# Kernel tuning notes

Measured on AMD Instinct MI355X. Metric: run time of the kernel, lower is better.

The kernel has to match this reference:

```python
import jax, jax.numpy as jnp
import numpy as np

N = 100_000      # total nodes in batched graph
NE = 800_000     # total edges
G = 1_000        # number of graphs in batch
V_DIM = 128      # node feat dim (== H_DIM, required by GRUCell usage)
E_DIM = 64       # edge feat dim
H_DIM = 128      # hidden dim
K_HEAD = 4       # multi-scale interaction heads


def _leaky(x):
    return jnp.where(x >= 0, x, 0.1 * x)


def _gru_cell(x, h, Wih, Whh, bih, bhh):
    # torch nn.GRUCell math; Wih/Whh stored as [in, 3*h] with (r,z,n) chunk order
    gi = x @ Wih + bih
    gh = h @ Whh + bhh
    ir, iz, inn = jnp.split(gi, 3, axis=-1)
    hr, hz, hn = jnp.split(gh, 3, axis=-1)
    r = jax.nn.sigmoid(ir + hr)
    z = jax.nn.sigmoid(iz + hz)
    n = jnp.tanh(inn + r * hn)
    return (1.0 - z) * n + z * h


def setup_inputs() -> dict:
    key = jax.random.key(0)
    ks = iter(jax.random.split(key, 48))
    def rn(shape, scale=0.05):
        return (jax.random.normal(next(ks), shape) * scale).astype(jnp.float32)
    inp = {}
    inp["v"] = rn((N, V_DIM), 1.0)
    inp["e"] = rn((NE, E_DIM), 1.0)
    inp["s"] = rn((G, V_DIM), 1.0)
    inp["edge_src"] = jax.random.randint(next(ks), (NE,), 0, N)
    inp["edge_dst"] = jax.random.randint(next(ks), (NE,), 0, N)
    inp["node_graph"] = jnp.repeat(jnp.arange(G), N // G)  # sorted segment ids
    # top-level linears (stored [in, out])
    inp["A_w"] = rn((V_DIM, H_DIM)); inp["A_b"] = rn((H_DIM,))
    inp["mA_w"] = rn((K_HEAD, V_DIM, H_DIM)); inp["mA_b"] = rn((K_HEAD, H_DIM))
    inp["mB_w"] = rn((K_HEAD, V_DIM, H_DIM)); inp["mB_b"] = rn((K_HEAD, H_DIM))
    inp["mC_w"] = rn((K_HEAD, H_DIM)); inp["mC_b"] = rn((K_HEAD,))
    inp["mD_w"] = rn((K_HEAD, V_DIM, H_DIM)); inp["mD_b"] = rn((K_HEAD, H_DIM))
    inp["B_w"] = rn((H_DIM * K_HEAD, H_DIM)); inp["B_b"] = rn((H_DIM,))
    inp["C_w"] = rn((V_DIM, H_DIM)); inp["C_b"] = rn((H_DIM,))
    inp["K_w"] = rn((E_DIM, H_DIM)); inp["K_b"] = rn((H_DIM,))
    inp["E_w"] = rn((H_DIM + V_DIM, H_DIM)); inp["E_b"] = rn((H_DIM,))
    for pfx in ("gm", "gs"):
        inp[pfx + "_A_w"] = rn((H_DIM, H_DIM)); inp[pfx + "_A_b"] = rn((H_DIM,))
        inp[pfx + "_B_w"] = rn((H_DIM, H_DIM)); inp[pfx + "_B_b"] = rn((H_DIM,))
        inp[pfx + "_Wih"] = rn((H_DIM, 3 * H_DIM)); inp[pfx + "_Whh"] = rn((H_DIM, 3 * H_DIM))
        inp[pfx + "_bih"] = rn((3 * H_DIM,)); inp[pfx + "_bhh"] = rn((3 * H_DIM,))
    return inp


def reference(v, e, s, edge_src, edge_dst, node_graph,
              A_w, A_b, mA_w, mA_b, mB_w, mB_b, mC_w, mC_b, mD_w, mD_b,
              B_w, B_b, C_w, C_b, K_w, K_b, E_w, E_b,
              gm_A_w, gm_A_b, gm_B_w, gm_B_b, gm_Wih, gm_Whh, gm_bih, gm_bhh,
              gs_A_w, gs_A_b, gs_B_w, gs_B_b, gs_Wih, gs_Whh, gs_bih, gs_bhh):
    # super -> super
    s2s = jnp.tanh(s @ A_w + A_b)                                       # [G,H]
    # multi-head node->super attention pooling (Multi_scale_interaction)
    d_node = jnp.tanh(jnp.einsum('nv,kvh->knh', v, mA_w) + mA_b[:, None, :])     # [K,N,H]
    d_super = jnp.tanh(jnp.einsum('gv,kvh->kgh', s, mB_w) + mB_b[:, None, :])    # [K,G,H]
    a = jnp.einsum('knh,kh->nk', d_node * d_super[:, node_graph, :], mC_w) + mC_b[None, :]  # [N,K]
    a_max = jax.ops.segment_max(a, node_graph, num_segments=G, indices_are_sorted=True)
    a_exp = jnp.exp(a - a_max[node_graph])
    denom = jax.ops.segment_sum(a_exp, node_graph, num_segments=G, indices_are_sorted=True)
    attn = a_exp / denom[node_graph]                                    # per-graph softmax, [N,K]
    d_v = jnp.einsum('nv,kvh->nkh', v, mD_w) + mD_b[None, :, :]         # [N,K,H]
    pooled = jax.ops.segment_sum(d_v * attn[:, :, None], node_graph, num_segments=G,
                                 indices_are_sorted=True)               # [G,K,H]
    m2s = jnp.tanh(pooled.reshape(G, K_HEAD * H_DIM) @ B_w + B_b)       # [G,H]
    # super -> node broadcast
    s2m = jnp.tanh(s @ C_w + C_b)[node_graph]                           # [N,H]
    # edge-wise message: leaky_relu(K(e) * v_src) summed into destination node
    ve = _leaky((e @ K_w + K_b) * v[edge_src])                          # [E,H]
    sve = jax.ops.segment_sum(ve, edge_dst, num_segments=N)             # [N,H]
    m2m = _leaky(jnp.concatenate([sve, v], axis=1) @ E_w + E_b)         # [N,H]
    # adaptive GRU gate: node update
    z_m = jax.nn.sigmoid(m2m @ gm_A_w + gm_A_b + s2m @ gm_B_w + gm_B_b)
    h_m = z_m * s2m + (1.0 - z_m) * m2m
    update_v = _gru_cell(v, h_m, gm_Wih, gm_Whh, gm_bih, gm_bhh)
    # adaptive GRU gate: supernode update
    z_s = jax.nn.sigmoid(s2s @ gs_A_w + gs_A_b + m2s @ gs_B_w + gs_B_b)
    h_s = z_s * m2s + (1.0 - z_s) * s2s
    update_s = _gru_cell(s, h_s, gs_Wih, gs_Whh, gs_bih, gs_bhh)
    return (update_v, update_s)
```

## Files before the change

### kernel.cpp

```cpp
#include <hip/hip_runtime.h>

#define NN   100000
#define NEDG 800000
#define NG   1000
#define HD   128
#define EDIM 64

typedef unsigned short u16;
typedef __bf16 bf16x8 __attribute__((ext_vector_type(8)));
typedef float f32x4 __attribute__((ext_vector_type(4)));

#define MFMA16(a, b, c) __builtin_amdgcn_mfma_f32_16x16x32_bf16(a, b, c, 0, 0, 0)

#define WS_E    0
#define WS_GA   4096
#define WS_WIH  6144
#define WS_WHH  12288
#define WS_MA0  18432
#define WS_KW   26624
#define WS_LANES 27648

#define BF(base, NTT, ks, nt, lane) \
    (*(const bf16x8*)(wsw + (size_t)((base) + (((ks) * (NTT) + (nt)) * 64 + (lane))) * 8))

__device__ __forceinline__ float sigmoidf_(float x) { return 1.0f / (1.0f + __expf(-x)); }
__device__ __forceinline__ float tanhf_(float x) {
    float ax = fabsf(x);
    float e  = __expf(-2.0f * ax);
    float t  = (1.0f - e) / (1.0f + e);
    return copysignf(t, x);
}
__device__ __forceinline__ float leaky_(float x) { return x >= 0.f ? x : 0.1f * x; }
__device__ __forceinline__ u16 f2bf(float x) {
    union { float f; unsigned u; } c; c.f = x;
    unsigned r = c.u + 0x7FFF + ((c.u >> 16) & 1);
    return (u16)(r >> 16);
}

__device__ __forceinline__ void stg4(u16* lds, int P, int r, int c0, float4 v4) {
    int byteoff = (c0 << 1) ^ ((r & 7) << 4);
    u16* p = lds + r * P + (byteoff >> 1);
    p[0] = f2bf(v4.x); p[1] = f2bf(v4.y); p[2] = f2bf(v4.z); p[3] = f2bf(v4.w);
}
__device__ __forceinline__ void stg1(u16* lds, int P, int r, int c, u16 val) {
    int byteoff = (c << 1) ^ ((r & 7) << 4);
    lds[r * P + (byteoff >> 1)] = val;
}
__device__ __forceinline__ bf16x8 ldA(const u16* lds, int P, int r, int ks, int hi) {
    int byteoff = (ks * 64 + (hi << 4)) ^ ((r & 7) << 4);
    return *(const bf16x8*)(lds + r * P + (byteoff >> 1));
}

__global__ __launch_bounds__(256) void wconv(
    const float* __restrict__ E_w, const float* __restrict__ gmA_w,
    const float* __restrict__ Wih, const float* __restrict__ Whh,
    const float* __restrict__ mA_w, const float* __restrict__ K_w,
    u16* __restrict__ dst)
{
    int t = blockIdx.x * 256 + threadIdx.x;
    if (t >= WS_LANES) return;
    const float* W; int N; int local;
    if (t < 4096)       { W = E_w;  N = 128; local = t; }
    else if (t < 6144)  { W = gmA_w; N = 128; local = t - 4096; }
    else if (t < 12288) { W = Wih;  N = 384; local = t - 6144; }
    else if (t < 18432) { W = Whh;  N = 384; local = t - 12288; }
    else if (t < 26624) { int k = (t - 18432) >> 11; W = mA_w + k * 128 * 128; N = 128; local = (t - 18432) & 2047; }
    else                { W = K_w;  N = 128; local = t - 26624; }
    int lane = local & 63;
    int fid  = local >> 6;
    int NT = N >> 4;
    int ks = fid / NT, nt = fid - ks * NT;
    int krow = ks * 32 + ((lane >> 4) << 3);
    int col  = nt * 16 + (lane & 15);
    u16* d = dst + (size_t)t * 8;
    #pragma unroll
    for (int j = 0; j < 8; j++) d[j] = f2bf(W[(size_t)(krow + j) * N + col]);
}

__global__ __launch_bounds__(128) void k1_graph(
    const float* __restrict__ s,
    const float* __restrict__ A_w, const float* __restrict__ A_b,
    const float* __restrict__ mB_w, const float* __restrict__ mB_b,
    const float* __restrict__ mC_w,
    const float* __restrict__ C_w, const float* __restrict__ C_b,
    const float* __restrict__ gmB_w, const float* __restrict__ gmA_b, const float* __restrict__ gmB_b,
    float* __restrict__ s2s, float* __restrict__ wkg,
    float* __restrict__ s2m_tab, float* __restrict__ t2)
{
    __shared__ float sm[HD];
    __shared__ float sm2[HD];
    const int g = blockIdx.x, t = threadIdx.x;
    sm[t] = s[g * HD + t];
    __syncthreads();
    {
        float a = 0.f;
        #pragma unroll 8
        for (int i = 0; i < HD; i++) a = fmaf(sm[i], A_w[i * HD + t], a);
        s2s[g * HD + t] = tanhf_(a + A_b[t]);
    }
    for (int k = 0; k < 4; k++) {
        float a = 0.f;
        const float* W = mB_w + k * HD * HD;
        #pragma unroll 8
        for (int i = 0; i < HD; i++) a = fmaf(sm[i], W[i * HD + t], a);
        float d = tanhf_(a + mB_b[k * HD + t]);
        wkg[(k * NG + g) * HD + t] = d * mC_w[k * HD + t];
    }
    float s2m;
    {
        float a = 0.f;
        #pragma unroll 8
        for (int i = 0; i < HD; i++) a = fmaf(sm[i], C_w[i * HD + t], a);
        s2m = tanhf_(a + C_b[t]);
        s2m_tab[g * HD + t] = s2m;
    }
    sm2[t] = s2m;
    __syncthreads();
    {
        float a = 0.f;
        #pragma unroll 8
        for (int i = 0; i < HD; i++) a = fmaf(sm2[i], gmB_w[i * HD + t], a);
        t2[g * HD + t] = a + gmA_b[t] + gmB_b[t];
    }
}

__global__ __launch_bounds__(256) void k2_ascore(
    const float* __restrict__ v, const int* __restrict__ ngr,
    const u16* __restrict__ wsw,
    const float* __restrict__ mA_b, const float* __restrict__ mC_b,
    const float* __restrict__ wkg,
    float* __restrict__ aexp, float* __restrict__ denom)
{
    __shared__ u16 VT[64 * 128];
    const int tid = threadIdx.x;
    const int n0 = blockIdx.x * 64;
    #pragma unroll
    for (int l = 0; l < 8; l++) {
        int i = tid + 256 * l;
        int r = i >> 5, c0 = (i & 31) << 2;
        int node = n0 + r;
        float4 vv = (node < NN) ? *(const float4*)(v + (size_t)node * HD + c0)
                                : make_float4(0.f, 0.f, 0.f, 0.f);
        stg4(VT, 128, r, c0, vv);
    }
    __syncthreads();
    const int lane = tid & 63, w = tid >> 6;
    const int l15 = lane & 15, hi = lane >> 4;
    const int rbase = w * 16;
    bf16x8 av[4];
    #pragma unroll
    for (int ks = 0; ks < 4; ks++) av[ks] = ldA(VT, 128, rbase + l15, ks, hi);
    int gq[4], nodeq[4];
    #pragma unroll
    for (int q = 0; q < 4; q++) {
        int nd = n0 + rbase + hi * 4 + q;
        nodeq[q] = nd;
        gq[q] = ngr[min(nd, NN - 1)];
    }
    for (int k = 0; k < 4; k++) {
        float rs[4] = {0.f, 0.f, 0.f, 0.f};
        const float* bias = mA_b + k * HD;
        #pragma unroll
        for (int nt = 0; nt < 8; nt++) {
            f32x4 acc = {0.f, 0.f, 0.f, 0.f};
            #pragma unroll
            for (int ks = 0; ks < 4; ks++)
                acc = MFMA16(av[ks], BF(WS_MA0 + k * 2048, 8, ks, nt, lane), acc);
            int col = nt * 16 + l15;
            float bb = bias[col];
            #pragma unroll
            for (int q = 0; q < 4; q++)
                rs[q] += tanhf_(acc[q] + bb) * wkg[((size_t)k * NG + gq[q]) * HD + col];
        }
        #pragma unroll
        for (int q = 0; q < 4; q++) {
            float x = rs[q];
            x += __shfl_xor(x, 1); x += __shfl_xor(x, 2);
            x += __shfl_xor(x, 4); x += __shfl_xor(x, 8);
            if (l15 == 0 && nodeq[q] < NN) {
                float ev = __expf(x + mC_b[k]);
                aexp[(size_t)nodeq[q] * 4 + k] = ev;
                atomicAdd(&denom[gq[q] * 4 + k], ev);
            }
        }
    }
}

__global__ __launch_bounds__(256) void k3_edge(
    const float* __restrict__ e, const float* __restrict__ v,
    const int* __restrict__ esrc, const int* __restrict__ edst,
    const u16* __restrict__ wsw, const float* __restrict__ K_b,
    float* __restrict__ sve)
{
    __shared__ u16 ET[64 * 64];
    const int tid = threadIdx.x;
    const int e0 = blockIdx.x * 64;
    #pragma unroll
    for (int l = 0; l < 4; l++) {
        int i = tid + 256 * l;
        int r = i >> 4, c0 = (i & 15) << 2;
        float4 ev4 = *(const float4*)(e + (size_t)(e0 + r) * EDIM + c0);
        stg4(ET, 64, r, c0, ev4);
    }
    __syncthreads();
    const int lane = tid & 63, w = tid >> 6;
    const int l15 = lane & 15, hi = lane >> 4;
    const int rbase = w * 16;
    bf16x8 ae[2];
    #pragma unroll
    for (int ks = 0; ks < 2; ks++) ae[ks] = ldA(ET, 64, rbase + l15, ks, hi);
    int sq[4], dq[4];
    #pragma unroll
    for (int q = 0; q < 4; q++) {
        int ei = e0 + rbase + hi * 4 + q;
        sq[q] = esrc[ei]; dq[q] = edst[ei];
    }
    #pragma unroll
    for (int nt = 0; nt < 8; nt++) {
        f32x4 acc = {0.f, 0.f, 0.f, 0.f};
        acc = MFMA16(ae[0], BF(WS_KW, 8, 0, nt, lane), acc);
        acc = MFMA16(ae[1], BF(WS_KW, 8, 1, nt, lane), acc);
        int col = nt * 16 + l15;
        float kb = K_b[col];
        #pragma unroll
        for (int q = 0; q < 4; q++) {
            float val = (acc[q] + kb) * v[(size_t)sq[q] * HD + col];
            val = leaky_(val);
            atomicAdd(&sve[(size_t)dq[q] * HD + col], val);
        }
    }
}

__global__ __launch_bounds__(256) void k4_vbar(
    const float* __restrict__ v, const int* __restrict__ ngr,
    const float* __restrict__ aexp, const float* __restrict__ denom,
    float* __restrict__ vbar)
{
    const int tid = threadIdx.x;
    const int d = tid & 127;
    const int hf = tid >> 7;
    const int n0 = blockIdx.x * 32 + hf * 16;
    int gcur = -1;
    float a0 = 0.f, a1 = 0.f, a2 = 0.f, a3 = 0.f;
    float4 rd = make_float4(0.f, 0.f, 0.f, 0.f);
    for (int nd = 0; nd < 16; nd++) {
        int n = n0 + nd;
        int g = ngr[n];
        if (g != gcur) {
            if (gcur >= 0) {
                atomicAdd(&vbar[(gcur * 4 + 0) * HD + d], a0);
                atomicAdd(&vbar[(gcur * 4 + 1) * HD + d], a1);
                atomicAdd(&vbar[(gcur * 4 + 2) * HD + d], a2);
                atomicAdd(&vbar[(gcur * 4 + 3) * HD + d], a3);
                a0 = a1 = a2 = a3 = 0.f;
            }
            float4 dn = *(const float4*)&denom[g * 4];
            rd = make_float4(1.f / dn.x, 1.f / dn.y, 1.f / dn.z, 1.f / dn.w);
            gcur = g;
        }
        float4 ae = *(const float4*)&aexp[n * 4];
        float vv = v[(size_t)n * HD + d];
        a0 = fmaf(ae.x * rd.x, vv, a0);
        a1 = fmaf(ae.y * rd.y, vv, a1);
        a2 = fmaf(ae.z * rd.z, vv, a2);
        a3 = fmaf(ae.w * rd.w, vv, a3);
    }
    atomicAdd(&vbar[(gcur * 4 + 0) * HD + d], a0);
    atomicAdd(&vbar[(gcur * 4 + 1) * HD + d], a1);
    atomicAdd(&vbar[(gcur * 4 + 2) * HD + d], a2);
    atomicAdd(&vbar[(gcur * 4 + 3) * HD + d], a3);
}

__global__ __launch_bounds__(128) void k5_super(
    const float* __restrict__ s, const float* __restrict__ vbar,
    const float* __restrict__ mD_w, const float* __restrict__ mD_b,
    const float* __restrict__ B_w, const float* __restrict__ B_b,
    const float* __restrict__ s2s,
    const float* __restrict__ gsA_w, const float* __restrict__ gsA_b,
    const float* __restrict__ gsB_w, const float* __restrict__ gsB_b,
    const float* __restrict__ gsWih, const float* __restrict__ gsWhh,
    const float* __restrict__ gsbih, const float* __restrict__ gsbhh,
    float* __restrict__ out_s)
{
    __shared__ float vb[4 * HD];
    __shared__ float p[4 * HD];
    __shared__ float m2s_l[HD];
    __shared__ float s2s_l[HD];
    __shared__ float hs_l[HD];
    __shared__ float srow[HD];
    const int g = blockIdx.x, t = threadIdx.x;
    #pragma unroll
    for (int l = 0; l < 4; l++) vb[t + HD * l] = vbar[(size_t)g * 4 * HD + t + HD * l];
    srow[t]  = s[g * HD + t];
    s2s_l[t] = s2s[g * HD + t];
    __syncthreads();
    for (int k = 0; k < 4; k++) {
        float a = 0.f;
        const float* W = mD_w + k * HD * HD;
        #pragma unroll 8
        for (int i = 0; i < HD; i++) a = fmaf(vb[k * HD + i], W[i * HD + t], a);
        p[k * HD + t] = a + mD_b[k * HD + t];
    }
    __syncthreads();
    float m2s;
    {
        float a = 0.f;
        #pragma unroll 8
        for (int j = 0; j < 4 * HD; j++) a = fmaf(p[j], B_w[j * HD + t], a);
        m2s = tanhf_(a + B_b[t]);
        m2s_l[t] = m2s;
    }
    __syncthreads();
    float hs;
    {
        float za = 0.f, zb = 0.f;
        #pragma unroll 8
        for (int i = 0; i < HD; i++) {
            za = fmaf(s2s_l[i], gsA_w[i * HD + t], za);
            zb = fmaf(m2s_l[i], gsB_w[i * HD + t], zb);
        }
        float z = sigmoidf_(za + gsA_b[t] + zb + gsB_b[t]);
        hs = z * m2s + (1.f - z) * s2s_l[t];
        hs_l[t] = hs;
    }
    __syncthreads();
    float gi0 = 0.f, gh0 = 0.f, gi1 = 0.f, gh1 = 0.f, gi2 = 0.f, gh2 = 0.f;
    #pragma unroll 4
    for (int i = 0; i < HD; i++) {
        float sv = srow[i], hv = hs_l[i];
        gi0 = fmaf(sv, gsWih[i * 384 + t], gi0);
        gh0 = fmaf(hv, gsWhh[i * 384 + t], gh0);
        gi1 = fmaf(sv, gsWih[i * 384 + 128 + t], gi1);
        gh1 = fmaf(hv, gsWhh[i * 384 + 128 + t], gh1);
        gi2 = fmaf(sv, gsWih[i * 384 + 256 + t], gi2);
        gh2 = fmaf(hv, gsWhh[i * 384 + 256 + t], gh2);
    }
    float r  = sigmoidf_(gi0 + gsbih[t] + gh0 + gsbhh[t]);
    float z2 = sigmoidf_(gi1 + gsbih[128 + t] + gh1 + gsbhh[128 + t]);
    float nn = tanhf_(gi2 + gsbih[256 + t] + r * (gh2 + gsbhh[256 + t]));
    out_s[g * HD + t] = (1.f - z2) * nn + z2 * hs;
}

__global__ __launch_bounds__(256) void k6_node(
    const float* __restrict__ v, const int* __restrict__ ngr,
    const float* __restrict__ sve, const u16* __restrict__ wsw,
    const float* __restrict__ E_b,
    const float* __restrict__ s2m_tab, const float* __restrict__ t2,
    const float* __restrict__ bih, const float* __restrict__ bhh,
    float* __restrict__ out_v)
{
    __shared__ u16 VT[64 * 128];
    __shared__ u16 ST[64 * 128];
    __shared__ u16 XT[64 * 128];
    const int tid = threadIdx.x;
    const int n0 = blockIdx.x * 64;
    #pragma unroll
    for (int l = 0; l < 8; l++) {
        int i = tid + 256 * l;
        int r = i >> 5, c0 = (i & 31) << 2;
        int node = n0 + r;
        float4 a = (node < NN) ? *(const float4*)(v   + (size_t)node * HD + c0) : make_float4(0.f, 0.f, 0.f, 0.f);
        float4 b = (node < NN) ? *(const float4*)(sve + (size_t)node * HD + c0) : make_float4(0.f, 0.f, 0.f, 0.f);
        stg4(VT, 128, r, c0, a);
        stg4(ST, 128, r, c0, b);
    }
    __syncthreads();
    const int lane = tid & 63, w = tid >> 6;
    const int l15 = lane & 15, hi = lane >> 4;
    const int rbase = w * 16;
    bf16x8 av[4], ax[4];
    #pragma unroll
    for (int ks = 0; ks < 4; ks++) {
        av[ks] = ldA(VT, 128, rbase + l15, ks, hi);
        ax[ks] = ldA(ST, 128, rbase + l15, ks, hi);
    }
    int gq[4], nodeq[4];
    #pragma unroll
    for (int q = 0; q < 4; q++) {
        int nd = n0 + rbase + hi * 4 + q;
        nodeq[q] = nd;
        gq[q] = ngr[min(nd, NN - 1)];
    }
    f32x4 hmf[8];
    #pragma unroll
    for (int nt = 0; nt < 8; nt++) {
        f32x4 acc = {0.f, 0.f, 0.f, 0.f};
        #pragma unroll
        for (int ks = 0; ks < 4; ks++) acc = MFMA16(ax[ks], BF(WS_E, 8, ks, nt, lane), acc);
        #pragma unroll
        for (int ks = 0; ks < 4; ks++) acc = MFMA16(av[ks], BF(WS_E, 8, 4 + ks, nt, lane), acc);
        int col = nt * 16 + l15;
        float eb = E_b[col];
        f32x4 m;
        #pragma unroll
        for (int q = 0; q < 4; q++) m[q] = leaky_(acc[q] + eb);
        hmf[nt] = m;
    }
    #pragma unroll
    for (int nt = 0; nt < 8; nt++) {
        int col = nt * 16 + l15;
        #pragma unroll
        for (int q = 0; q < 4; q++) stg1(ST, 128, rbase + hi * 4 + q, col, f2bf(hmf[nt][q]));
    }
    bf16x8 am[4];
    #pragma unroll
    for (int ks = 0; ks < 4; ks++) am[ks] = ldA(ST, 128, rbase + l15, ks, hi);
    #pragma unroll
    for (int nt = 0; nt < 8; nt++) {
        f32x4 acc = {0.f, 0.f, 0.f, 0.f};
        #pragma unroll
        for (int ks = 0; ks < 4; ks++) acc = MFMA16(am[ks], BF(WS_GA, 8, ks, nt, lane), acc);
        int col = nt * 16 + l15;
        #pragma unroll
        for (int q = 0; q < 4; q++) {
            int g = gq[q];
            float z  = sigmoidf_(acc[q] + t2[(size_t)g * HD + col]);
            float hm = z * s2m_tab[(size_t)g * HD + col] + (1.f - z) * hmf[nt][q];
            hmf[nt][q] = hm;
            stg1(XT, 128, rbase + hi * 4 + q, col, f2bf(hm));
        }
    }
    bf16x8 ah[4];
    #pragma unroll
    for (int ks = 0; ks < 4; ks++) ah[ks] = ldA(XT, 128, rbase + l15, ks, hi);
    #pragma unroll
    for (int nt = 0; nt < 8; nt++) {
        f32x4 air = {0.f,0.f,0.f,0.f}, aiz = {0.f,0.f,0.f,0.f}, ain = {0.f,0.f,0.f,0.f};
        f32x4 ahr = {0.f,0.f,0.f,0.f}, ahz = {0.f,0.f,0.f,0.f}, ahn = {0.f,0.f,0.f,0.f};
        #pragma unroll
        for (int ks = 0; ks < 4; ks++) {
            air = MFMA16(av[ks], BF(WS_WIH, 24, ks, nt,      lane), air);
            ahr = MFMA16(ah[ks], BF(WS_WHH, 24, ks, nt,      lane), ahr);
            aiz = MFMA16(av[ks], BF(WS_WIH, 24, ks, nt + 8,  lane), aiz);
            ahz = MFMA16(ah[ks], BF(WS_WHH, 24, ks, nt + 8,  lane), ahz);
            ain = MFMA16(av[ks], BF(WS_WIH, 24, ks, nt + 16, lane), ain);
            ahn = MFMA16(ah[ks], BF(WS_WHH, 24, ks, nt + 16, lane), ahn);
        }
        int col = nt * 16 + l15;
        float br  = bih[col] + bhh[col];
        float bz  = bih[HD + col] + bhh[HD + col];
        float bi3 = bih[2 * HD + col];
        float bh3 = bhh[2 * HD + col];
        #pragma unroll
        for (int q = 0; q < 4; q++) {
            float r   = sigmoidf_(air[q] + ahr[q] + br);
            float z   = sigmoidf_(aiz[q] + ahz[q] + bz);
            float nnv = tanhf_(ain[q] + bi3 + r * (ahn[q] + bh3));
            if (nodeq[q] < NN)
                out_v[(size_t)nodeq[q] * HD + col] = (1.f - z) * nnv + z * hmf[nt][q];
        }
    }
}

extern "C" void kernel_launch(void* const* d_in, const int* in_sizes, int n_in,
                              void* d_out, int out_size, void* d_ws, size_t ws_size,
                              hipStream_t stream)
{
    const float* v    = (const float*)d_in[0];
    const float* e    = (const float*)d_in[1];
    const float* s    = (const float*)d_in[2];
    const int*   esrc = (const int*)d_in[3];
    const int*   edst = (const int*)d_in[4];
    const int*   ngr  = (const int*)d_in[5];
    const float* A_w  = (const float*)d_in[6];
    const float* A_b  = (const float*)d_in[7];
    const float* mA_w = (const float*)d_in[8];
    const float* mA_b = (const float*)d_in[9];
    const float* mB_w = (const float*)d_in[10];
    const float* mB_b = (const float*)d_in[11];
    const float* mC_w = (const float*)d_in[12];
    const float* mC_b = (const float*)d_in[13];
    const float* mD_w = (const float*)d_in[14];
    const float* mD_b = (const float*)d_in[15];
    const float* B_w  = (const float*)d_in[16];
    const float* B_b  = (const float*)d_in[17];
    const float* C_w  = (const float*)d_in[18];
    const float* C_b  = (const float*)d_in[19];
    const float* K_w  = (const float*)d_in[20];
    const float* K_b  = (const float*)d_in[21];
    const float* E_w  = (const float*)d_in[22];
    const float* E_b  = (const float*)d_in[23];
    const float* gmA_w = (const float*)d_in[24];
    const float* gmA_b = (const float*)d_in[25];
    const float* gmB_w = (const float*)d_in[26];
    const float* gmB_b = (const float*)d_in[27];
    const float* gmWih = (const float*)d_in[28];
    const float* gmWhh = (const float*)d_in[29];
    const float* gmbih = (const float*)d_in[30];
    const float* gmbhh = (const float*)d_in[31];
    const float* gsA_w = (const float*)d_in[32];
    const float* gsA_b = (const float*)d_in[33];
    const float* gsB_w = (const float*)d_in[34];
    const float* gsB_b = (const float*)d_in[35];
    const float* gsWih = (const float*)d_in[36];
    const float* gsWhh = (const float*)d_in[37];
    const float* gsbih = (const float*)d_in[38];
    const float* gsbhh = (const float*)d_in[39];

    float* ws      = (float*)d_ws;
    float* sve     = ws;
    float* aexp    = sve + 12800000;
    float* denom   = aexp + 400000;
    float* wkg     = denom + 4000;
    float* s2s     = wkg + 512000;
    float* s2m_tab = s2s + 128000;
    float* t2      = s2m_tab + 128000;
    float* vbar    = t2 + 128000;
    u16*   wswz    = (u16*)(vbar + 512000);

    hipMemsetAsync(sve, 0, (size_t)12800000 * 4, stream);
    hipMemsetAsync(denom, 0, (size_t)4000 * 4, stream);
    hipMemsetAsync(vbar, 0, (size_t)512000 * 4, stream);

    float* out_v = (float*)d_out;
    float* out_s = out_v + (size_t)NN * HD;

    wconv<<<(WS_LANES + 255) / 256, 256, 0, stream>>>(E_w, gmA_w, gmWih, gmWhh, mA_w, K_w, wswz);
    k1_graph<<<NG, 128, 0, stream>>>(s, A_w, A_b, mB_w, mB_b, mC_w, C_w, C_b,
                                     gmB_w, gmA_b, gmB_b, s2s, wkg, s2m_tab, t2);
    k2_ascore<<<(NN + 63) / 64, 256, 0, stream>>>(v, ngr, wswz, mA_b, mC_b, wkg, aexp, denom);
    k3_edge<<<NEDG / 64, 256, 0, stream>>>(e, v, esrc, edst, wswz, K_b, sve);
    k4_vbar<<<NN / 32, 256, 0, stream>>>(v, ngr, aexp, denom, vbar);
    k5_super<<<NG, 128, 0, stream>>>(s, vbar, mD_w, mD_b, B_w, B_b, s2s,
                                     gsA_w, gsA_b, gsB_w, gsB_b,
                                     gsWih, gsWhh, gsbih, gsbhh, out_s);
    k6_node<<<(NN + 63) / 64, 256, 0, stream>>>(v, ngr, sve, wswz, E_b, s2m_tab, t2,
                                                gmbih, gmbhh, out_v);
}
```

Before: 794.7 us.

## Sort edges by destination and combine atomics for consecutive same-destination edges

Builds a counting-sort permutation of edges by destination (histogram, three-stage scan, atomic scatter) on every call. The edge kernel then gathers its edge rows through that permutation and adds up runs of equal destinations within each lane's four edges before issuing atomics. The aim is fewer and more localized atomicAdds into sve. The cost is six extra launches, a serial scan, and scattered reads of the e rows. The sorted path runs only when the workspace is large enough; otherwise it falls back to the old kernel.

```diff
diff --git a/kernel.cpp b/kernel.cpp
--- a/kernel.cpp
+++ b/kernel.cpp
@@ -77,6 +77,61 @@
     for (int j = 0; j < 8; j++) d[j] = f2bf(W[(size_t)(krow + j) * N + col]);
 }
 
+__global__ __launch_bounds__(256) void k_hist(const int* __restrict__ edst, int* __restrict__ cnt) {
+    int i = blockIdx.x * 256 + threadIdx.x;
+    if (i < NEDG) atomicAdd(&cnt[edst[i]], 1);
+}
+
+__global__ __launch_bounds__(256) void k_scan1(const int* __restrict__ cnt,
+                                               int* __restrict__ excl, int* __restrict__ bsum) {
+    __shared__ int sd[256];
+    int t = threadIdx.x, b = blockIdx.x;
+    int base = b * 1024 + t * 4;
+    int v0 = (base + 0 < NN) ? cnt[base + 0] : 0;
+    int v1 = (base + 1 < NN) ? cnt[base + 1] : 0;
+    int v2 = (base + 2 < NN) ? cnt[base + 2] : 0;
+    int v3 = (base + 3 < NN) ? cnt[base + 3] : 0;
+    int s = v0 + v1 + v2 + v3;
+    sd[t] = s;
+    __syncthreads();
+    for (int off = 1; off < 256; off <<= 1) {
+        int x = (t >= off) ? sd[t - off] : 0;
+        __syncthreads();
+        sd[t] += x;
+        __syncthreads();
+    }
+    int incl = sd[t];
+    int ex = incl - s;
+    if (base + 0 < NN) excl[base + 0] = ex;
+    if (base + 1 < NN) excl[base + 1] = ex + v0;
+    if (base + 2 < NN) excl[base + 2] = ex + v0 + v1;
+    if (base + 3 < NN) excl[base + 3] = ex + v0 + v1 + v2;
+    if (t == 255) bsum[b] = incl;
+}
+
+#define NSCB 98
+__global__ void k_scan2(int* __restrict__ bsum) {
+    if (threadIdx.x == 0 && blockIdx.x == 0) {
+        int run = 0;
+        for (int i = 0; i < NSCB; i++) { int t = bsum[i]; bsum[i] = run; run += t; }
+    }
+}
+
+__global__ __launch_bounds__(256) void k_scan3(const int* __restrict__ excl,
+                                               const int* __restrict__ bsum, int* __restrict__ start) {
+    int i = blockIdx.x * 256 + threadIdx.x;
+    if (i < NN) start[i] = excl[i] + bsum[i >> 10];
+}
+
+__global__ __launch_bounds__(256) void k_scatter(const int* __restrict__ edst,
+                                                 int* __restrict__ start, int* __restrict__ perm) {
+    int i = blockIdx.x * 256 + threadIdx.x;
+    if (i < NEDG) {
+        int pos = atomicAdd(&start[edst[i]], 1);
+        perm[pos] = i;
+    }
+}
+
 __global__ __launch_bounds__(128) void k1_graph(
     const float* __restrict__ s,
     const float* __restrict__ A_w, const float* __restrict__ A_b,
@@ -186,20 +241,24 @@
     }
 }
 
-__global__ __launch_bounds__(256) void k3_edge(
+__global__ __launch_bounds__(256) void k3_edge_sorted(
     const float* __restrict__ e, const float* __restrict__ v,
     const int* __restrict__ esrc, const int* __restrict__ edst,
+    const int* __restrict__ perm,
     const u16* __restrict__ wsw, const float* __restrict__ K_b,
     float* __restrict__ sve)
 {
     __shared__ u16 ET[64 * 64];
+    __shared__ int pid[64];
     const int tid = threadIdx.x;
     const int e0 = blockIdx.x * 64;
+    if (tid < 64) pid[tid] = perm[e0 + tid];
+    __syncthreads();
     #pragma unroll
     for (int l = 0; l < 4; l++) {
         int i = tid + 256 * l;
         int r = i >> 4, c0 = (i & 15) << 2;
-        float4 ev4 = *(const float4*)(e + (size_t)(e0 + r) * EDIM + c0);
+        float4 ev4 = *(const float4*)(e + (size_t)pid[r] * EDIM + c0);
         stg4(ET, 64, r, c0, ev4);
     }
     __syncthreads();
@@ -212,7 +271,7 @@
     int sq[4], dq[4];
     #pragma unroll
     for (int q = 0; q < 4; q++) {
-        int ei = e0 + rbase + hi * 4 + q;
+        int ei = pid[rbase + hi * 4 + q];
         sq[q] = esrc[ei]; dq[q] = edst[ei];
     }
     #pragma unroll
@@ -222,10 +281,59 @@
         acc = MFMA16(ae[1], BF(WS_KW, 8, 1, nt, lane), acc);
         int col = nt * 16 + l15;
         float kb = K_b[col];
+        float vals[4];
+        #pragma unroll
+        for (int q = 0; q < 4; q++)
+            vals[q] = leaky_((acc[q] + kb) * v[(size_t)sq[q] * HD + col]);
+        float a = vals[0];
+        #pragma unroll
+        for (int q = 1; q < 4; q++) {
+            if (dq[q] == dq[q - 1]) a += vals[q];
+            else { atomicAdd(&sve[(size_t)dq[q - 1] * HD + col], a); a = vals[q]; }
+        }
+        atomicAdd(&sve[(size_t)dq[3] * HD + col], a);
+    }
+}
+
+__global__ __launch_bounds__(256) void k3_edge_unsorted(
+    const float* __restrict__ e, const float* __restrict__ v,
+    const int* __restrict__ esrc, const int* __restrict__ edst,
+    const u16* __restrict__ wsw, const float* __restrict__ K_b,
+    float* __restrict__ sve)
+{
+    __shared__ u16 ET[64 * 64];
+    const int tid = threadIdx.x;
+    const int e0 = blockIdx.x * 64;
+    #pragma unroll
+    for (int l = 0; l < 4; l++) {
+        int i = tid + 256 * l;
+        int r = i >> 4, c0 = (i & 15) << 2;
+        float4 ev4 = *(const float4*)(e + (size_t)(e0 + r) * EDIM + c0);
+        stg4(ET, 64, r, c0, ev4);
+    }
+    __syncthreads();
+    const int lane = tid & 63, w = tid >> 6;
+    const int l15 = lane & 15, hi = lane >> 4;
+    const int rbase = w * 16;
+    bf16x8 ae[2];
+    #pragma unroll
+    for (int ks = 0; ks < 2; ks++) ae[ks] = ldA(ET, 64, rbase + l15, ks, hi);
+    int sq[4], dq[4];
+    #pragma unroll
+    for (int q = 0; q < 4; q++) {
+        int ei = e0 + rbase + hi * 4 + q;
+        sq[q] = esrc[ei]; dq[q] = edst[ei];
+    }
+    #pragma unroll
+    for (int nt = 0; nt < 8; nt++) {
+        f32x4 acc = {0.f, 0.f, 0.f, 0.f};
+        acc = MFMA16(ae[0], BF(WS_KW, 8, 0, nt, lane), acc);
+        acc = MFMA16(ae[1], BF(WS_KW, 8, 1, nt, lane), acc);
+        int col = nt * 16 + l15;
+        float kb = K_b[col];
         #pragma unroll
         for (int q = 0; q < 4; q++) {
-            float val = (acc[q] + kb) * v[(size_t)sq[q] * HD + col];
-            val = leaky_(val);
+            float val = leaky_((acc[q] + kb) * v[(size_t)sq[q] * HD + col]);
             atomicAdd(&sve[(size_t)dq[q] * HD + col], val);
         }
     }
@@ -507,6 +615,14 @@
     float* t2      = s2m_tab + 128000;
     float* vbar    = t2 + 128000;
     u16*   wswz    = (u16*)(vbar + 512000);
+    int*   isc     = (int*)(wswz + 221184);
+    int*   cnt     = isc;
+    int*   excl    = cnt + 100000;
+    int*   bsum    = excl + 100000;
+    int*   startp  = bsum + 128;
+    int*   perm    = startp + 100000;
+    const size_t NEED = ((size_t)(perm + 800000 - (int*)d_ws)) * 4;
+    const bool do_sort = ws_size >= NEED;
 
     hipMemsetAsync(sve, 0, (size_t)12800000 * 4, stream);
     hipMemsetAsync(denom, 0, (size_t)4000 * 4, stream);
@@ -518,8 +634,20 @@
     wconv<<<(WS_LANES + 255) / 256, 256, 0, stream>>>(E_w, gmA_w, gmWih, gmWhh, mA_w, K_w, wswz);
     k1_graph<<<NG, 128, 0, stream>>>(s, A_w, A_b, mB_w, mB_b, mC_w, C_w, C_b,
                                      gmB_w, gmA_b, gmB_b, s2s, wkg, s2m_tab, t2);
+    if (do_sort) {
+        hipMemsetAsync(cnt, 0, (size_t)100000 * 4, stream);
+        k_hist<<<(NEDG + 255) / 256, 256, 0, stream>>>(edst, cnt);
+        k_scan1<<<NSCB, 256, 0, stream>>>(cnt, excl, bsum);
+        k_scan2<<<1, 64, 0, stream>>>(bsum);
+        k_scan3<<<(NN + 255) / 256, 256, 0, stream>>>(excl, bsum, startp);
+        k_scatter<<<(NEDG + 255) / 256, 256, 0, stream>>>(edst, startp, perm);
+    }
     k2_ascore<<<(NN + 63) / 64, 256, 0, stream>>>(v, ngr, wswz, mA_b, mC_b, wkg, aexp, denom);
-    k3_edge<<<NEDG / 64, 256, 0, stream>>>(e, v, esrc, edst, wswz, K_b, sve);
+    if (do_sort) {
+        k3_edge_sorted<<<NEDG / 64, 256, 0, stream>>>(e, v, esrc, edst, perm, wswz, K_b, sve);
+    } else {
+        k3_edge_unsorted<<<NEDG / 64, 256, 0, stream>>>(e, v, esrc, edst, wswz, K_b, sve);
+    }
     k4_vbar<<<NN / 32, 256, 0, stream>>>(v, ngr, aexp, denom, vbar);
     k5_super<<<NG, 128, 0, stream>>>(s, vbar, mD_w, mD_b, B_w, B_b, s2s,
                                      gsA_w, gsA_b, gsB_w, gsB_b,
```

New measurement: 778.6 us. 2.0% less time.
